# Optimization experiments

Hardware: AMD Instinct MI355X
Metric: run time of the kernel (lower is better)

## Reference

```python
import jax, jax.numpy as jnp
import numpy as np

D_MODEL = 1024
NUM_HEADS = 16
HEAD_DIM = D_MODEL // NUM_HEADS


def setup_inputs() -> dict:
    key = jax.random.key(0)
    ks = jax.random.split(key, 10)
    B, SQ, SKV = 2, 2048, 2048
    s = 1.0 / np.sqrt(D_MODEL)
    inp = {
        "query": jax.random.normal(ks[0], (B, SQ, D_MODEL), jnp.float32),
        "key_value": jax.random.normal(ks[1], (B, SKV, D_MODEL), jnp.float32),
        "Wq": jax.random.normal(ks[2], (D_MODEL, D_MODEL), jnp.float32) * s,
        "bq": jnp.zeros((D_MODEL,), jnp.float32),
        "Wk": jax.random.normal(ks[3], (D_MODEL, D_MODEL), jnp.float32) * s,
        "bk": jnp.zeros((D_MODEL,), jnp.float32),
        "Wv": jax.random.normal(ks[4], (D_MODEL, D_MODEL), jnp.float32) * s,
        "bv": jnp.zeros((D_MODEL,), jnp.float32),
        "Wo": jax.random.normal(ks[5], (D_MODEL, D_MODEL), jnp.float32) * s,
        "bo": jnp.zeros((D_MODEL,), jnp.float32),
    }
    return inp


def reference(query, key_value, Wq, bq, Wk, bk, Wv, bv, Wo, bo):
    B, SQ, _ = query.shape
    SKV = key_value.shape[1]
    # projections (torch Linear: x @ W^T + b)
    Q = query @ Wq.T + bq
    K = key_value @ Wk.T + bk
    V = key_value @ Wv.T + bv
    # [B, H, S, Dh]
    Q = Q.reshape(B, SQ, NUM_HEADS, HEAD_DIM).transpose(0, 2, 1, 3)
    K = K.reshape(B, SKV, NUM_HEADS, HEAD_DIM).transpose(0, 2, 1, 3)
    V = V.reshape(B, SKV, NUM_HEADS, HEAD_DIM).transpose(0, 2, 1, 3)
    scores = jnp.einsum("bhqd,bhkd->bhqk", Q, K) / np.sqrt(HEAD_DIM)
    # causal mask: position q may attend to kv positions <= q
    causal = jnp.tril(jnp.ones((SQ, SKV), bool))  # True = keep
    scores = jnp.where(causal[None, None], scores, -jnp.inf)
    attn = jax.nn.softmax(scores, axis=-1)
    # dropout is identity in eval mode
    out = jnp.einsum("bhqk,bhkd->bhqd", attn, V)
    out = out.transpose(0, 2, 1, 3).reshape(B, SQ, D_MODEL)
    return out @ Wo.T + bo
```

## Files before the change

kernel.cpp:

```cpp
#include <hip/hip_runtime.h>
#include <hip/hip_bf16.h>
#include <cstdint>

#define DM 1024
#define HEADS 16
#define DH 64
#define SEQ 2048
#define BATCH 2

typedef __attribute__((ext_vector_type(8))) short bf16x8;
typedef __attribute__((ext_vector_type(4))) float f32x4;
typedef __attribute__((ext_vector_type(16))) float f32x16;
typedef __attribute__((ext_vector_type(2))) unsigned int u32x2;
typedef __attribute__((ext_vector_type(4))) unsigned int u32x4;

#define SCALE2 0.18033688011112042f

static __device__ __forceinline__ unsigned short f2bf(float f) {
    unsigned u = __builtin_bit_cast(unsigned, f);
    u = u + 0x7fffu + ((u >> 16) & 1u);
    return (unsigned short)(u >> 16);
}

__global__ __launch_bounds__(256) void cast_all_k(
    const float* __restrict__ q, const float* __restrict__ kv,
    const float* __restrict__ wq, const float* __restrict__ wk,
    const float* __restrict__ wv, const float* __restrict__ wo,
    unsigned short* __restrict__ qb, unsigned short* __restrict__ kvb,
    unsigned short* __restrict__ wqb, unsigned short* __restrict__ wkb,
    unsigned short* __restrict__ wvb, unsigned short* __restrict__ wob)
{
    int blk = blockIdx.x;
    const float* s; unsigned short* d; int base;
    if (blk < 2048)      { s = q;  d = qb;  base = 0; }
    else if (blk < 4096) { s = kv; d = kvb; base = 2048; }
    else if (blk < 4608) { s = wq; d = wqb; base = 4096; }
    else if (blk < 5120) { s = wk; d = wkb; base = 4608; }
    else if (blk < 5632) { s = wv; d = wvb; base = 5120; }
    else                 { s = wo; d = wob; base = 5632; }
    int i = ((blk - base) * 256 + threadIdx.x) * 8;
    float4 a = *(const float4*)(s + i);
    float4 b2 = *(const float4*)(s + i + 4);
    ushort4 o0, o1;
    o0.x = f2bf(a.x);  o0.y = f2bf(a.y);  o0.z = f2bf(a.z);  o0.w = f2bf(a.w);
    o1.x = f2bf(b2.x); o1.y = f2bf(b2.y); o1.z = f2bf(b2.z); o1.w = f2bf(b2.w);
    *(ushort4*)(d + i) = o0;
    *(ushort4*)(d + i + 4) = o1;
}

template<int EPI>
__global__ __launch_bounds__(256) void gemm_nt(
    const unsigned short* __restrict__ A,
    const unsigned short* __restrict__ Bw,
    const float* __restrict__ biasA,
    const float* __restrict__ biasB,
    void* __restrict__ out0,
    void* __restrict__ out1,
    int M, int N, int K)
{
    constexpr int BK = 64;
    __shared__ alignas(16) unsigned short As[64 * BK];
    __shared__ alignas(16) unsigned short Bs[128 * BK];

    const int t = threadIdx.x;
    const int lane = t & 63;
    const int w = t >> 6;
    const int wn = w * 32;
    const int lr = lane & 15, lg = lane >> 4;
    const int m0 = blockIdx.x * 64, n0 = blockIdx.y * 128;

    f32x4 acc[4][2] = {};

    const int srow = t >> 3;
    const int schunk = t & 7;

    for (int kt = 0; kt < K; kt += BK) {
#pragma unroll
        for (int c = 0; c < 2; c++) {
            int row = srow + c * 32;
            int gc = schunk ^ (row & 7);
            __builtin_amdgcn_global_load_lds(
                (const __attribute__((address_space(1))) unsigned int*)(A + (size_t)(m0 + row) * K + kt + gc * 8),
                (__attribute__((address_space(3))) unsigned int*)(&As[row * BK + schunk * 8]), 16, 0, 0);
        }
#pragma unroll
        for (int c = 0; c < 4; c++) {
            int row = srow + c * 32;
            int gc = schunk ^ (row & 7);
            __builtin_amdgcn_global_load_lds(
                (const __attribute__((address_space(1))) unsigned int*)(Bw + (size_t)(n0 + row) * K + kt + gc * 8),
                (__attribute__((address_space(3))) unsigned int*)(&Bs[row * BK + schunk * 8]), 16, 0, 0);
        }
        __syncthreads();
#pragma unroll
        for (int kk = 0; kk < 2; kk++) {
            bf16x8 af[4], bfr[2];
#pragma unroll
            for (int i = 0; i < 4; i++)
                af[i] = *(const bf16x8*)(&As[(i * 16 + lr) * BK + (((kk * 4 + lg) ^ (lr & 7))) * 8]);
#pragma unroll
            for (int jj = 0; jj < 2; jj++)
                bfr[jj] = *(const bf16x8*)(&Bs[(wn + jj * 16 + lr) * BK + (((kk * 4 + lg) ^ (lr & 7))) * 8]);
#pragma unroll
            for (int i = 0; i < 4; i++)
#pragma unroll
                for (int jj = 0; jj < 2; jj++)
                    acc[i][jj] = __builtin_amdgcn_mfma_f32_16x16x32_bf16(af[i], bfr[jj], acc[i][jj], 0, 0, 0);
        }
        __syncthreads();
    }

    if constexpr (EPI == 0) {
        unsigned short* C = (unsigned short*)out0;
#pragma unroll
        for (int i = 0; i < 4; i++) {
            int rbase = m0 + i * 16 + lg * 4;
#pragma unroll
            for (int jj = 0; jj < 2; jj++) {
                int col = n0 + wn + jj * 16 + lr;
                float bv = biasA[col];
#pragma unroll
                for (int r = 0; r < 4; r++)
                    C[(size_t)(rbase + r) * 1024 + col] = f2bf((acc[i][jj][r] + bv) * SCALE2);
            }
        }
    } else if constexpr (EPI == 1) {
        if (n0 < 1024) {
            unsigned short* C = (unsigned short*)out0;
#pragma unroll
            for (int i = 0; i < 4; i++) {
                int rbase = m0 + i * 16 + lg * 4;
#pragma unroll
                for (int jj = 0; jj < 2; jj++) {
                    int col = n0 + wn + jj * 16 + lr;
                    float bv = biasA[col];
#pragma unroll
                    for (int r = 0; r < 4; r++)
                        C[(size_t)(rbase + r) * 1024 + col] = f2bf(acc[i][jj][r] + bv);
                }
            }
        } else {
            unsigned short* C = (unsigned short*)out1;
            int bidx = m0 >> 11;
#pragma unroll
            for (int i = 0; i < 4; i++) {
                int s0 = (m0 & 2047) + i * 16 + lg * 4;
#pragma unroll
                for (int jj = 0; jj < 2; jj++) {
                    int nv = n0 - 1024 + wn + jj * 16 + lr;
                    float bv = biasB[nv];
                    int hh = nv >> 6, dd = nv & 63;
                    ushort4 st;
                    st.x = f2bf(acc[i][jj][0] + bv);
                    st.y = f2bf(acc[i][jj][1] + bv);
                    st.z = f2bf(acc[i][jj][2] + bv);
                    st.w = f2bf(acc[i][jj][3] + bv);
                    *(ushort4*)(C + ((size_t)((bidx * HEADS + hh) * DH + dd)) * SEQ + s0) = st;
                }
            }
        }
    } else {
        float* C = (float*)out0;
#pragma unroll
        for (int i = 0; i < 4; i++) {
            int rbase = m0 + i * 16 + lg * 4;
#pragma unroll
            for (int jj = 0; jj < 2; jj++) {
                int col = n0 + wn + jj * 16 + lr;
                float bv = biasA[col];
#pragma unroll
                for (int r = 0; r < 4; r++)
                    C[(size_t)(rbase + r) * 1024 + col] = acc[i][jj][r] + bv;
            }
        }
    }
}

__global__ __launch_bounds__(512, 2) void attn_k(
    const unsigned short* __restrict__ Qp,
    const unsigned short* __restrict__ Kp,
    const unsigned short* __restrict__ Vt,
    unsigned short* __restrict__ Ctx)
{
    const int lane = threadIdx.x & 63;
    const int w = threadIdx.x >> 6;
    const int j = blockIdx.x;
    const int h = blockIdx.y, b = blockIdx.z;
    const int qt = (w < 4) ? (j * 4 + w) : (63 - j * 4 - (w & 3));
    const int q0 = qt * 32;
    const int lq = lane & 31;
    const int hi = lane >> 5;
    const int qq = q0 + lq;
    constexpr float THR = 11.5f;

    bf16x8 Qf[4];
    {
        const unsigned short* qb = Qp + (size_t)(b * SEQ + qq) * DM + h * DH + hi * 8;
#pragma unroll
        for (int d = 0; d < 4; d++) Qf[d] = *(const bf16x8*)(qb + d * 16);
    }

    const unsigned short* kbase = Kp + ((size_t)(b * SEQ + lq)) * DM + h * DH + hi * 8;
    const unsigned short* vbase = Vt + ((size_t)((b * HEADS + h) * DH) + lq) * SEQ + hi * 8;

    const int nt = qt + 1;
    const int nA = nt >> 1;
    const int nB = nt - nA;

    f32x16 oA0 = {}, oA1 = {}, oB0 = {}, oB1 = {};
    float mA = -1e30f, lA = 0.f, mB = -1e30f, lB = 0.f;
    bf16x8 KA[4], VA[4], KB[4], VB[4];

    const int qmh0 = qq - 4 * hi;

    auto loadKV = [&](bf16x8 (&Kc)[4], bf16x8 (&Vc)[4], int kb) {
        const unsigned short* kp = kbase + (size_t)kb * DM;
#pragma unroll
        for (int d = 0; d < 4; d++) Kc[d] = *(const bf16x8*)(kp + d * 16);
        const unsigned short* vp = vbase + kb;
#pragma unroll
        for (int s = 0; s < 2; s++)
#pragma unroll
            for (int dt = 0; dt < 2; dt++)
                Vc[s * 2 + dt] = *(const bf16x8*)(vp + (size_t)dt * 32 * SEQ + s * 16);
    };

    if (nA > 0) loadKV(KA, VA, 0);
    loadKV(KB, VB, nA * 32);

    auto step = [&](bf16x8 (&Kc)[4], bf16x8 (&Vc)[4], f32x16& o0, f32x16& o1,
                    float& m_run, float& l_run, int kb, bool pf) {
        bf16x8 Kn[4], Vn[4];
        if (pf) {
            const unsigned short* kp = kbase + (size_t)(kb + 32) * DM;
#pragma unroll
            for (int d = 0; d < 4; d++) Kn[d] = *(const bf16x8*)(kp + d * 16);
            const unsigned short* vp = vbase + kb + 32;
#pragma unroll
            for (int s = 0; s < 2; s++)
#pragma unroll
                for (int dt = 0; dt < 2; dt++)
                    Vn[s * 2 + dt] = *(const bf16x8*)(vp + (size_t)dt * 32 * SEQ + s * 16);
        }

        f32x16 sa = {};
#pragma unroll
        for (int d = 0; d < 4; d++)
            sa = __builtin_amdgcn_mfma_f32_32x32x16_bf16(Kc[d], Qf[d], sa, 0, 0, 0);

        const int qmh = qmh0 - kb;
#pragma unroll
        for (int r = 0; r < 16; r++) {
            int kvl = (r & 3) + 8 * (r >> 2);
            sa[r] = (kvl <= qmh) ? sa[r] : -1e30f;
        }
        float mx[8];
#pragma unroll
        for (int r = 0; r < 8; r++) mx[r] = fmaxf(sa[2 * r], sa[2 * r + 1]);
#pragma unroll
        for (int r = 0; r < 4; r++) mx[r] = fmaxf(mx[r], mx[r + 4]);
        mx[0] = fmaxf(mx[0], mx[2]);
        mx[1] = fmaxf(mx[1], mx[3]);
        float mloc = fmaxf(mx[0], mx[1]);
        mloc = fmaxf(mloc, __shfl_xor(mloc, 32));

        if (!__all(mloc - m_run <= THR)) {
            float m_new = fmaxf(m_run, mloc);
            float sf = __builtin_amdgcn_exp2f(m_run - m_new);
            l_run *= sf;
#pragma unroll
            for (int r = 0; r < 16; r++) { o0[r] *= sf; o1[r] *= sf; }
            m_run = m_new;
        }

        float ps = 0.f;
        unsigned c[8];
#pragma unroll
        for (int i = 0; i < 8; i++) {
            float p0 = __builtin_amdgcn_exp2f(sa[2 * i] - m_run);
            float p1 = __builtin_amdgcn_exp2f(sa[2 * i + 1] - m_run);
            ps += p0 + p1;
            unsigned pk;
            asm("v_cvt_pk_bf16_f32 %0, %1, %2" : "=v"(pk) : "v"(p0), "v"(p1));
            c[i] = pk;
        }
        ps += __shfl_xor(ps, 32);
        l_run += ps;

        u32x2 r02 = __builtin_amdgcn_permlane32_swap(c[0], c[2], false, false);
        u32x2 r13 = __builtin_amdgcn_permlane32_swap(c[1], c[3], false, false);
        u32x2 r46 = __builtin_amdgcn_permlane32_swap(c[4], c[6], false, false);
        u32x2 r57 = __builtin_amdgcn_permlane32_swap(c[5], c[7], false, false);
        u32x4 w0 = {r02.x, r13.x, r02.y, r13.y};
        u32x4 w1 = {r46.x, r57.x, r46.y, r57.y};
        bf16x8 Pb0 = __builtin_bit_cast(bf16x8, w0);
        bf16x8 Pb1 = __builtin_bit_cast(bf16x8, w1);

        o0 = __builtin_amdgcn_mfma_f32_32x32x16_bf16(Vc[0], Pb0, o0, 0, 0, 0);
        o1 = __builtin_amdgcn_mfma_f32_32x32x16_bf16(Vc[1], Pb0, o1, 0, 0, 0);
        o0 = __builtin_amdgcn_mfma_f32_32x32x16_bf16(Vc[2], Pb1, o0, 0, 0, 0);
        o1 = __builtin_amdgcn_mfma_f32_32x32x16_bf16(Vc[3], Pb1, o1, 0, 0, 0);

        if (pf) {
#pragma unroll
            for (int d = 0; d < 4; d++) Kc[d] = Kn[d];
#pragma unroll
            for (int s = 0; s < 4; s++) Vc[s] = Vn[s];
        }
    };

    for (int i = 0; i < nA; i++) {
        step(KA, VA, oA0, oA1, mA, lA, i * 32, i + 1 < nA);
        step(KB, VB, oB0, oB1, mB, lB, (nA + i) * 32, i + 1 < nB);
    }
    if (nB > nA)
        step(KB, VB, oB0, oB1, mB, lB, (nt - 1) * 32, false);

    float m = fmaxf(mA, mB);
    float cA = __builtin_amdgcn_exp2f(mA - m);
    float cB = __builtin_amdgcn_exp2f(mB - m);
    float l = lA * cA + lB * cB;
    float inv = 1.0f / l;
    float fA = cA * inv, fB = cB * inv;

    unsigned short* cb = Ctx + (size_t)(b * SEQ + qq) * DM + h * DH + hi * 4;
#pragma unroll
    for (int g = 0; g < 4; g++) {
        ushort4 s0, s1;
        s0.x = f2bf(oA0[4 * g + 0] * fA + oB0[4 * g + 0] * fB);
        s0.y = f2bf(oA0[4 * g + 1] * fA + oB0[4 * g + 1] * fB);
        s0.z = f2bf(oA0[4 * g + 2] * fA + oB0[4 * g + 2] * fB);
        s0.w = f2bf(oA0[4 * g + 3] * fA + oB0[4 * g + 3] * fB);
        s1.x = f2bf(oA1[4 * g + 0] * fA + oB1[4 * g + 0] * fB);
        s1.y = f2bf(oA1[4 * g + 1] * fA + oB1[4 * g + 1] * fB);
        s1.z = f2bf(oA1[4 * g + 2] * fA + oB1[4 * g + 2] * fB);
        s1.w = f2bf(oA1[4 * g + 3] * fA + oB1[4 * g + 3] * fB);
        *(ushort4*)(cb + g * 8) = s0;
        *(ushort4*)(cb + 32 + g * 8) = s1;
    }
}

extern "C" void kernel_launch(void* const* d_in, const int* in_sizes, int n_in,
                              void* d_out, int out_size, void* d_ws, size_t ws_size,
                              hipStream_t stream)
{
    const float* query = (const float*)d_in[0];
    const float* keyv  = (const float*)d_in[1];
    const float* Wq = (const float*)d_in[2];
    const float* bq = (const float*)d_in[3];
    const float* Wk = (const float*)d_in[4];
    const float* bk = (const float*)d_in[5];
    const float* Wv = (const float*)d_in[6];
    const float* bv = (const float*)d_in[7];
    const float* Wo = (const float*)d_in[8];
    const float* bo = (const float*)d_in[9];
    float* out = (float*)d_out;

    const int M = BATCH * SEQ;
    char* ws = (char*)d_ws;
    size_t off = 0;
    auto alloc = [&](size_t elems) { unsigned short* p = (unsigned short*)(ws + off); off += elems * 2; return p; };
    unsigned short* qb  = alloc((size_t)M * DM);
    unsigned short* kvb = alloc((size_t)M * DM);
    unsigned short* wqb = alloc((size_t)DM * DM);
    unsigned short* wkb = alloc((size_t)DM * DM);
    unsigned short* wvb = alloc((size_t)DM * DM);
    unsigned short* wob = alloc((size_t)DM * DM);
    unsigned short* Qp  = alloc((size_t)M * DM);
    unsigned short* Kp  = alloc((size_t)M * DM);
    unsigned short* Vt  = alloc((size_t)M * DM);
    unsigned short* Ctx = alloc((size_t)M * DM);

    cast_all_k<<<6144, 256, 0, stream>>>(query, keyv, Wq, Wk, Wv, Wo,
                                         qb, kvb, wqb, wkb, wvb, wob);

    gemm_nt<0><<<dim3(M / 64, 8),  256, 0, stream>>>(qb,  wqb, bq, nullptr, Qp, nullptr, M, DM, DM);
    gemm_nt<1><<<dim3(M / 64, 16), 256, 0, stream>>>(kvb, wkb, bk, bv,      Kp, Vt,      M, 2 * DM, DM);

    attn_k<<<dim3(8, HEADS, BATCH), 512, 0, stream>>>(Qp, Kp, Vt, Ctx);

    gemm_nt<2><<<dim3(M / 64, 8),  256, 0, stream>>>(Ctx, wob, bo, nullptr, out, nullptr, M, DM, DM);
}
```

Baseline: 139.2 us.

## Split each query tile's KV range across two waves and merge via LDS

Each 32-row query tile now goes to a pair of waves. They take alternating even and odd KV blocks, so each wave holds one softmax state and half the registers. The partial outputs and max/sum stats are exchanged through shared memory and merged, and each wave writes half of the head-dim columns. The grid doubles to 16 blocks per head with launch bounds raised to 4 blocks per SM, and V is no longer prefetched, only K. This aims to raise occupancy and parallelism, at the cost of a __syncthreads, LDS traffic and less latency hiding on V loads.

```diff
diff --git a/kernel.cpp b/kernel.cpp
--- a/kernel.cpp
+++ b/kernel.cpp
@@ -1,6 +1,7 @@
 #include <hip/hip_runtime.h>
 #include <hip/hip_bf16.h>
 #include <cstdint>
+#include <type_traits>
 
 #define DM 1024
 #define HEADS 16
@@ -176,21 +177,32 @@
     }
 }
 
-__global__ __launch_bounds__(512, 2) void attn_k(
+__global__ __launch_bounds__(512, 4) void attn_k(
     const unsigned short* __restrict__ Qp,
     const unsigned short* __restrict__ Kp,
     const unsigned short* __restrict__ Vt,
     unsigned short* __restrict__ Ctx)
 {
+    __shared__ float oBuf[8][64][18];
+    __shared__ float2 mlBuf[8][64];
+
     const int lane = threadIdx.x & 63;
     const int w = threadIdx.x >> 6;
     const int j = blockIdx.x;
     const int h = blockIdx.y, b = blockIdx.z;
-    const int qt = (w < 4) ? (j * 4 + w) : (63 - j * 4 - (w & 3));
+
+    int qt;
+    if (w < 2)      qt = 63 - 2 * j;
+    else if (w < 4) qt = 62 - 2 * j;
+    else if (w < 6) qt = 2 * j;
+    else            qt = 2 * j + 1;
+    const int half = w & 1;
     const int q0 = qt * 32;
     const int lq = lane & 31;
     const int hi = lane >> 5;
     const int qq = q0 + lq;
+    const int nt = qt + 1;
+    const int n = (nt + 1 - half) >> 1;
     constexpr float THR = 11.5f;
 
     bf16x8 Qf[4];
@@ -203,44 +215,36 @@
     const unsigned short* kbase = Kp + ((size_t)(b * SEQ + lq)) * DM + h * DH + hi * 8;
     const unsigned short* vbase = Vt + ((size_t)((b * HEADS + h) * DH) + lq) * SEQ + hi * 8;
 
-    const int nt = qt + 1;
-    const int nA = nt >> 1;
-    const int nB = nt - nA;
-
-    f32x16 oA0 = {}, oA1 = {}, oB0 = {}, oB1 = {};
-    float mA = -1e30f, lA = 0.f, mB = -1e30f, lB = 0.f;
-    bf16x8 KA[4], VA[4], KB[4], VB[4];
+    f32x16 o0 = {}, o1 = {};
+    float m_run = -1e30f, l_run = 0.f;
+    bf16x8 Kc[4];
+
+    {
+        const unsigned short* kp = kbase + (size_t)(half * 32) * DM;
+#pragma unroll
+        for (int d = 0; d < 4; d++) Kc[d] = *(const bf16x8*)(kp + d * 16);
+    }
 
     const int qmh0 = qq - 4 * hi;
 
-    auto loadKV = [&](bf16x8 (&Kc)[4], bf16x8 (&Vc)[4], int kb) {
-        const unsigned short* kp = kbase + (size_t)kb * DM;
-#pragma unroll
-        for (int d = 0; d < 4; d++) Kc[d] = *(const bf16x8*)(kp + d * 16);
-        const unsigned short* vp = vbase + kb;
-#pragma unroll
-        for (int s = 0; s < 2; s++)
-#pragma unroll
-            for (int dt = 0; dt < 2; dt++)
-                Vc[s * 2 + dt] = *(const bf16x8*)(vp + (size_t)dt * 32 * SEQ + s * 16);
-    };
-
-    if (nA > 0) loadKV(KA, VA, 0);
-    loadKV(KB, VB, nA * 32);
-
-    auto step = [&](bf16x8 (&Kc)[4], bf16x8 (&Vc)[4], f32x16& o0, f32x16& o1,
-                    float& m_run, float& l_run, int kb, bool pf) {
-        bf16x8 Kn[4], Vn[4];
-        if (pf) {
-            const unsigned short* kp = kbase + (size_t)(kb + 32) * DM;
+    auto body = [&](int kbt, auto PF) {
+        constexpr bool pf = PF.value;
+        const int kb = kbt * 32;
+
+        bf16x8 Vc[4];
+        {
+            const unsigned short* vp = vbase + kb;
+#pragma unroll
+            for (int s = 0; s < 2; s++)
+#pragma unroll
+                for (int dt = 0; dt < 2; dt++)
+                    Vc[s * 2 + dt] = *(const bf16x8*)(vp + (size_t)dt * 32 * SEQ + s * 16);
+        }
+        bf16x8 Kn[4];
+        if constexpr (pf) {
+            const unsigned short* kp = kbase + (size_t)(kb + 64) * DM;
 #pragma unroll
             for (int d = 0; d < 4; d++) Kn[d] = *(const bf16x8*)(kp + d * 16);
-            const unsigned short* vp = vbase + kb + 32;
-#pragma unroll
-            for (int s = 0; s < 2; s++)
-#pragma unroll
-                for (int dt = 0; dt < 2; dt++)
-                    Vn[s * 2 + dt] = *(const bf16x8*)(vp + (size_t)dt * 32 * SEQ + s * 16);
         }
 
         f32x16 sa = {};
@@ -301,42 +305,46 @@
         o0 = __builtin_amdgcn_mfma_f32_32x32x16_bf16(Vc[2], Pb1, o0, 0, 0, 0);
         o1 = __builtin_amdgcn_mfma_f32_32x32x16_bf16(Vc[3], Pb1, o1, 0, 0, 0);
 
-        if (pf) {
+        if constexpr (pf) {
 #pragma unroll
             for (int d = 0; d < 4; d++) Kc[d] = Kn[d];
-#pragma unroll
-            for (int s = 0; s < 4; s++) Vc[s] = Vn[s];
         }
     };
 
-    for (int i = 0; i < nA; i++) {
-        step(KA, VA, oA0, oA1, mA, lA, i * 32, i + 1 < nA);
-        step(KB, VB, oB0, oB1, mB, lB, (nA + i) * 32, i + 1 < nB);
-    }
-    if (nB > nA)
-        step(KB, VB, oB0, oB1, mB, lB, (nt - 1) * 32, false);
-
-    float m = fmaxf(mA, mB);
-    float cA = __builtin_amdgcn_exp2f(mA - m);
-    float cB = __builtin_amdgcn_exp2f(mB - m);
-    float l = lA * cA + lB * cB;
+    for (int i = 0; i + 1 < n; i++)
+        body(2 * i + half, std::true_type{});
+    if (n > 0)
+        body(2 * (n - 1) + half, std::false_type{});
+
+    {
+        float* ob = &oBuf[w][lane][0];
+        const f32x16& oX = (w & 1) ? o0 : o1;
+#pragma unroll
+        for (int e = 0; e < 8; e++)
+            *(float2*)(ob + 2 * e) = make_float2(oX[2 * e], oX[2 * e + 1]);
+        mlBuf[w][lane] = make_float2(m_run, l_run);
+    }
+    __syncthreads();
+
+    float2 mlO = mlBuf[w ^ 1][lane];
+    const float* obO = &oBuf[w ^ 1][lane][0];
+    float mM = fmaxf(m_run, mlO.x);
+    float cS = __builtin_amdgcn_exp2f(m_run - mM);
+    float cO = __builtin_amdgcn_exp2f(mlO.x - mM);
+    float l = l_run * cS + mlO.y * cO;
     float inv = 1.0f / l;
-    float fA = cA * inv, fB = cB * inv;
-
-    unsigned short* cb = Ctx + (size_t)(b * SEQ + qq) * DM + h * DH + hi * 4;
+    float fS = cS * inv, fO = cO * inv;
+
+    const f32x16& oSelf = (w & 1) ? o1 : o0;
+    unsigned short* cb = Ctx + (size_t)(b * SEQ + qq) * DM + h * DH + hi * 4 + (w & 1) * 32;
 #pragma unroll
     for (int g = 0; g < 4; g++) {
-        ushort4 s0, s1;
-        s0.x = f2bf(oA0[4 * g + 0] * fA + oB0[4 * g + 0] * fB);
-        s0.y = f2bf(oA0[4 * g + 1] * fA + oB0[4 * g + 1] * fB);
-        s0.z = f2bf(oA0[4 * g + 2] * fA + oB0[4 * g + 2] * fB);
-        s0.w = f2bf(oA0[4 * g + 3] * fA + oB0[4 * g + 3] * fB);
-        s1.x = f2bf(oA1[4 * g + 0] * fA + oB1[4 * g + 0] * fB);
-        s1.y = f2bf(oA1[4 * g + 1] * fA + oB1[4 * g + 1] * fB);
-        s1.z = f2bf(oA1[4 * g + 2] * fA + oB1[4 * g + 2] * fB);
-        s1.w = f2bf(oA1[4 * g + 3] * fA + oB1[4 * g + 3] * fB);
-        *(ushort4*)(cb + g * 8) = s0;
-        *(ushort4*)(cb + 32 + g * 8) = s1;
+        ushort4 st;
+        st.x = f2bf(oSelf[4 * g + 0] * fS + obO[4 * g + 0] * fO);
+        st.y = f2bf(oSelf[4 * g + 1] * fS + obO[4 * g + 1] * fO);
+        st.z = f2bf(oSelf[4 * g + 2] * fS + obO[4 * g + 2] * fO);
+        st.w = f2bf(oSelf[4 * g + 3] * fS + obO[4 * g + 3] * fO);
+        *(ushort4*)(cb + g * 8) = st;
     }
 }
 
@@ -377,7 +385,7 @@
     gemm_nt<0><<<dim3(M / 64, 8),  256, 0, stream>>>(qb,  wqb, bq, nullptr, Qp, nullptr, M, DM, DM);
     gemm_nt<1><<<dim3(M / 64, 16), 256, 0, stream>>>(kvb, wkb, bk, bv,      Kp, Vt,      M, 2 * DM, DM);
 
-    attn_k<<<dim3(8, HEADS, BATCH), 512, 0, stream>>>(Qp, Kp, Vt, Ctx);
+    attn_k<<<dim3(16, HEADS, BATCH), 512, 0, stream>>>(Qp, Kp, Vt, Ctx);
 
     gemm_nt<2><<<dim3(M / 64, 8),  256, 0, stream>>>(Ctx, wob, bo, nullptr, out, nullptr, M, DM, DM);
 }
```

Measured after the change: 142.0 us. +2.1%, slower.
